# Kernel optimization log

Measured on AMD Instinct MI355X. Metric: run time of the kernel, lower is better.

Reference implementation:

```python
import jax, jax.numpy as jnp
import numpy as np

B, N_X, N_A, DIM = 2, 2048, 2048, 1024
HEADS, DH = 16, 64
SEG = 256
ROPE_THETA = 10000.0


def mh_rmsnorm(t, gamma):
    # t: [b,h,n,d], gamma: [h,1,d]; F.normalize(dim=-1) * gamma * sqrt(d)
    norm = jnp.linalg.norm(t, axis=-1, keepdims=True)
    return t / jnp.clip(norm, 1e-12) * gamma * (DH ** 0.5)


def apply_rope(t):
    # t: [b,h,n,d]; GPT-NeoX style half-split rotary over packed positions
    n = t.shape[2]
    half = DH // 2
    inv_freq = ROPE_THETA ** (-jnp.arange(0, half, dtype=jnp.float32) / half)
    freqs = jnp.arange(n, dtype=jnp.float32)[:, None] * inv_freq[None, :]  # [n, half]
    cos, sin = jnp.cos(freqs), jnp.sin(freqs)
    t1, t2 = t[..., :half], t[..., half:]
    return jnp.concatenate([t1 * cos - t2 * sin, t2 * cos + t1 * sin], axis=-1)


def infini_attention(q, k, v, beta):
    # q,k,v: [b,h,n,d]; causal local attention per segment + recurrent linear memory
    b, h, n, d = q.shape
    s = n // SEG
    scale = d ** -0.5
    gate = jax.nn.sigmoid(beta).reshape(1, h, 1, 1)
    causal = jnp.tril(jnp.ones((SEG, SEG), dtype=bool))

    def to_segs(t):  # -> [s, b, h, SEG, d]
        return jnp.moveaxis(t.reshape(b, h, s, SEG, d), 2, 0)

    qs, ks, vs = to_segs(q), to_segs(k), to_segs(v)

    def step(carry, inp):
        M, z = carry  # M: [b,h,d,d], z: [b,h,d]
        q_s, k_s, v_s = inp
        sq = jax.nn.elu(q_s) + 1.0
        sk = jax.nn.elu(k_s) + 1.0
        # memory retrieval
        num = jnp.einsum('bhld,bhde->bhle', sq, M)
        den = jnp.einsum('bhld,bhd->bhl', sq, z)[..., None] + 1e-6
        a_mem = num / den
        # local causal attention within segment
        scores = jnp.einsum('bhid,bhjd->bhij', q_s, k_s) * scale
        scores = jnp.where(causal, scores, -jnp.inf)
        a_loc = jnp.einsum('bhij,bhjd->bhid', jax.nn.softmax(scores, axis=-1), v_s)
        out = gate * a_mem + (1.0 - gate) * a_loc
        # memory update
        M = M + jnp.einsum('bhld,bhle->bhde', sk, v_s)
        z = z + sk.sum(axis=2)
        return (M, z), out

    M0 = jnp.zeros((b, h, d, d), dtype=q.dtype)
    z0 = jnp.zeros((b, h, d), dtype=q.dtype)
    _, outs = jax.lax.scan(step, (M0, z0), (qs, ks, vs))  # [s,b,h,SEG,d]
    return jnp.moveaxis(outs, 0, 2).reshape(b, h, n, d)


def setup_inputs() -> dict:
    key = jax.random.key(0)
    ks = jax.random.split(key, 4)
    scale = DIM ** -0.5
    x = jax.random.normal(ks[0], (B, N_X, DIM), dtype=jnp.float32)
    a = jax.random.normal(ks[1], (B, N_A, DIM), dtype=jnp.float32)
    w_qkv_x = jax.random.normal(ks[2], (DIM, 3 * HEADS * DH), dtype=jnp.float32) * scale
    w_qkv_a = jax.random.normal(ks[3], (DIM, 3 * HEADS * DH), dtype=jnp.float32) * scale
    g = lambda: jnp.ones((HEADS, 1, DH), dtype=jnp.float32)
    beta = jnp.zeros((HEADS,), dtype=jnp.float32)
    return {"x": x, "a": a, "w_qkv_x": w_qkv_x, "w_qkv_a": w_qkv_a,
            "gq_x": g(), "gk_x": g(), "gq_a": g(), "gk_a": g(), "beta": beta}


def _split_heads(t):
    b, n, _ = t.shape
    q, k, v = jnp.split(t, 3, axis=-1)
    r = lambda u: u.reshape(b, n, HEADS, DH).transpose(0, 2, 1, 3)
    return r(q), r(k), r(v)


def reference(x, a, w_qkv_x, w_qkv_a, gq_x, gk_x, gq_a, gk_a, beta):
    q_x, k_x, v_x = _split_heads(x @ w_qkv_x)
    q_a, k_a, v_a = _split_heads(a @ w_qkv_a)
    q_x, k_x = mh_rmsnorm(q_x, gq_x), mh_rmsnorm(k_x, gk_x)
    q_a, k_a = mh_rmsnorm(q_a, gq_a), mh_rmsnorm(k_a, gk_a)
    # pack: a-stream first, then x-stream (matches pack([._a, ._x]))
    q = jnp.concatenate([q_a, q_x], axis=2)
    k = jnp.concatenate([k_a, k_x], axis=2)
    v = jnp.concatenate([v_a, v_x], axis=2)
    q, k = apply_rope(q), apply_rope(k)
    out = infini_attention(q, k, v, beta)  # [b,h,n_a+n_x,d]
    out_a, out_x = out[:, :, :N_A], out[:, :, N_A:]
    merge = lambda t: t.transpose(0, 2, 1, 3).reshape(t.shape[0], t.shape[2], HEADS * DH)
    return merge(out_x), merge(out_a)
```

## Files before the change

### kernel.cpp

```cpp
#include <hip/hip_runtime.h>

#define HEADS 16
#define DH    64
#define NA    2048
#define NX    2048
#define NTOT  4096
#define DIMK  1024
#define NQKV  3072
#define SEG   256
#define NSEG  16

typedef float          f32x4  __attribute__((ext_vector_type(4)));
typedef short          bf16x8 __attribute__((ext_vector_type(8)));
typedef unsigned int   u32x4  __attribute__((ext_vector_type(4)));

__device__ __forceinline__ unsigned short f2bf(float f){
  unsigned int u = __builtin_bit_cast(unsigned int, f);
  unsigned int r = 0x7fffu + ((u >> 16) & 1u);
  return (unsigned short)((u + r) >> 16);
}
__device__ __forceinline__ float bf2f(unsigned short u){
  return __builtin_bit_cast(float, ((unsigned int)u) << 16);
}

__global__ __launch_bounds__(256) void zero_kernel(float* __restrict__ out, int n){
  int i = blockIdx.x * 256 + threadIdx.x;
  if (i < n) out[i] = 0.f;
}

__global__ __launch_bounds__(256) void cvt_kernel(const float* __restrict__ src,
                                                  unsigned short* __restrict__ dst, int n4){
  int i = blockIdx.x * 256 + threadIdx.x;
  if (i >= n4) return;
  float4 v = ((const float4*)src)[i];
  ushort4 o;
  o.x = f2bf(v.x); o.y = f2bf(v.y); o.z = f2bf(v.z); o.w = f2bf(v.w);
  ((ushort4*)dst)[i] = o;
}

__global__ __launch_bounds__(256) void wtr_kernel(const float* __restrict__ W,
                                                  unsigned short* __restrict__ WT){
  __shared__ float tile[32][33];
  int c0 = blockIdx.x * 32, k0 = blockIdx.y * 32;
  int tx = threadIdx.x, ty = threadIdx.y;
  #pragma unroll
  for (int i = 0; i < 32; i += 8) tile[ty+i][tx] = W[(size_t)(k0+ty+i)*NQKV + c0 + tx];
  __syncthreads();
  #pragma unroll
  for (int i = 0; i < 32; i += 8) WT[(size_t)(c0+ty+i)*DIMK + k0 + tx] = f2bf(tile[tx][ty+i]);
}

__global__ __launch_bounds__(256) void rope_tab_kernel(float* __restrict__ tab){
  const int idx = blockIdx.x * 256 + threadIdx.x;
  const int n = idx >> 5, d = idx & 31;
  const float ang = (float)n * expf(-(float)d * 0.28782313662425572f);
  float sn, cs;
  sincosf(ang, &sn, &cs);
  float2 p; p.x = cs; p.y = sn;
  ((float2*)tab)[idx] = p;
}

__global__ __launch_bounds__(256,2) void gemm_qkv_kernel(
    const unsigned short* __restrict__ Xb, const unsigned short* __restrict__ Ab,
    const unsigned short* __restrict__ WTx, const unsigned short* __restrict__ WTa,
    unsigned short* __restrict__ qb, unsigned short* __restrict__ kb,
    unsigned short* __restrict__ vt,
    const float* __restrict__ gqx, const float* __restrict__ gkx,
    const float* __restrict__ gqa, const float* __restrict__ gka,
    const float* __restrict__ tab)
{
  __shared__ __align__(16) unsigned short As0[128*32];
  __shared__ __align__(16) unsigned short Bs0[128*32];
  __shared__ __align__(16) unsigned short As1[128*32];
  __shared__ __align__(16) unsigned short Bs1[128*32];

  const int bid = blockIdx.x;
  const int lid = (bid & 7) * 192 + (bid >> 3);
  const int strm = lid / 768;
  const int rem  = lid - strm * 768;
  const int c0 = (rem >> 5) * 128;
  const int m0 = (rem & 31) * 128;

  const unsigned short* Xp = strm ? Ab  : Xb;
  const unsigned short* Wp = strm ? WTa : WTx;
  const float* gq = strm ? gqa : gqx;
  const float* gk = strm ? gka : gkx;
  const int n_off = strm ? 0 : NA;

  const int tid  = threadIdx.x;
  const int lane = tid & 63, w = tid >> 6;
  const int wr = w >> 1, wc = w & 1;
  const int li = lane & 15, lg = lane >> 4;

  const int srow = lane >> 2;
  const int sslot = lane & 3;
  const int sswz = sslot ^ (srow & 3) ^ ((srow >> 2) & 3);
  const int rswz = (li & 3) ^ ((li >> 2) & 3);

  f32x4 acc[4][4] = {};

  auto stage = [&](unsigned short* AsX, unsigned short* BsX, int kk){
    #pragma unroll
    for (int jj = 0; jj < 2; jj++){
      const int j = 2*w + jj;
      const int r = j*16 + srow;
      __builtin_amdgcn_global_load_lds(
        (const __attribute__((address_space(1))) unsigned int*)(Xp + (size_t)(m0+r)*DIMK + kk + sswz*8),
        (__attribute__((address_space(3))) unsigned int*)(AsX + j*512), 16, 0, 0);
      __builtin_amdgcn_global_load_lds(
        (const __attribute__((address_space(1))) unsigned int*)(Wp + (size_t)(c0+r)*DIMK + kk + sswz*8),
        (__attribute__((address_space(3))) unsigned int*)(BsX + j*512), 16, 0, 0);
    }
  };
  auto compute = [&](const unsigned short* AsX, const unsigned short* BsX){
    bf16x8 af[4], bf[4];
    const int slot = (lg ^ rswz) * 8;
    #pragma unroll
    for (int m = 0; m < 4; m++)
      af[m] = *(const bf16x8*)(&AsX[(wr*64 + m*16 + li)*32 + slot]);
    #pragma unroll
    for (int n = 0; n < 4; n++)
      bf[n] = *(const bf16x8*)(&BsX[(wc*64 + n*16 + li)*32 + slot]);
    #pragma unroll
    for (int m = 0; m < 4; m++)
      #pragma unroll
      for (int n = 0; n < 4; n++)
        acc[m][n] = __builtin_amdgcn_mfma_f32_16x16x32_bf16(af[m], bf[n], acc[m][n], 0, 0, 0);
  };

  stage(As0, Bs0, 0);
  __syncthreads();
  for (int t = 0; t < 32; t += 2){
    stage(As1, Bs1, (t+1)*32);
    compute(As0, Bs0);
    __syncthreads();
    if (t + 2 < 32) stage(As0, Bs0, (t+2)*32);
    compute(As1, Bs1);
    __syncthreads();
  }

  const int colbase = c0 + wc*64;
  const int which = colbase >> 10;
  const int h = (colbase >> 6) & 15;

  if (which < 2){
    const float* gv = (which == 0) ? gq : gk;
    unsigned short* dstb = (which == 0) ? qb : kb;
    float gl[4];
    #pragma unroll
    for (int n = 0; n < 4; n++) gl[n] = gv[h*64 + n*16 + li];
    #pragma unroll
    for (int m = 0; m < 4; m++){
      #pragma unroll
      for (int r = 0; r < 4; r++){
        float ss = acc[m][0][r]*acc[m][0][r] + acc[m][1][r]*acc[m][1][r]
                 + acc[m][2][r]*acc[m][2][r] + acc[m][3][r]*acc[m][3][r];
        ss += __shfl_xor(ss, 1, 64);
        ss += __shfl_xor(ss, 2, 64);
        ss += __shfl_xor(ss, 4, 64);
        ss += __shfl_xor(ss, 8, 64);
        const float sc = 8.0f / fmaxf(sqrtf(ss), 1e-12f);
        float v0 = acc[m][0][r]*sc*gl[0], v1 = acc[m][1][r]*sc*gl[1];
        float v2 = acc[m][2][r]*sc*gl[2], v3 = acc[m][3][r]*sc*gl[3];
        const int row = m0 + wr*64 + m*16 + lg*4 + r;
        const int bb = row >> 11, nn = row & 2047;
        const int n_g = nn + n_off;
        const float2 cs0 = ((const float2*)tab)[n_g*32 + li];
        const float2 cs1 = ((const float2*)tab)[n_g*32 + 16 + li];
        const float o0 = v0*cs0.x - v2*cs0.y;
        const float o1 = v1*cs1.x - v3*cs1.y;
        const float o2 = v2*cs0.x + v0*cs0.y;
        const float o3 = v3*cs1.x + v1*cs1.y;
        unsigned short* drow = dstb + ((size_t)(bb*HEADS + h)*NTOT + (size_t)n_g)*64;
        drow[li]      = f2bf(o0);
        drow[16 + li] = f2bf(o1);
        drow[32 + li] = f2bf(o2);
        drow[48 + li] = f2bf(o3);
      }
    }
  } else {
    #pragma unroll
    for (int m = 0; m < 4; m++){
      #pragma unroll
      for (int r = 0; r < 4; r++){
        const int row = m0 + wr*64 + m*16 + lg*4 + r;
        const int bb = row >> 11, nn = row & 2047;
        const int n_g = nn + n_off;
        unsigned short* vbase = vt + (size_t)(bb*HEADS + h)*DH*NTOT + n_g;
        #pragma unroll
        for (int n = 0; n < 4; n++)
          vbase[(size_t)(n*16 + li)*NTOT] = f2bf(acc[m][n][r]);
      }
    }
  }
}

__global__ __launch_bounds__(256,2) void segG_kernel(const unsigned short* __restrict__ kb,
                                                     const unsigned short* __restrict__ vt,
                                                     float* __restrict__ G, float* __restrict__ zc){
  __shared__ unsigned short skT[64*264];
  __shared__ unsigned short Vts[64*264];
  const int blk = blockIdx.x;
  const int bh = blk >> 4, s = blk & 15;
  const int tid = threadIdx.x;
  const int w = tid >> 6, lane = tid & 63;
  const int li = lane & 15, lg = lane >> 4;
  const size_t segoffb = ((size_t)bh * NTOT + (size_t)s * SEG) * DH;

  #pragma unroll
  for (int it = 0; it < 8; it++){
    const int idx = tid + it*256;
    const int e = idx >> 5, jc = idx & 31;
    *(u32x4*)(Vts + e*264 + jc*8) =
      *(const u32x4*)(vt + (size_t)bh*DH*NTOT + (size_t)e*NTOT + s*SEG + jc*8);
  }
  #pragma unroll
  for (int it = 0; it < 8; it++){
    const int idx = tid + it*256;
    const int l = idx >> 3, dc = idx & 7;
    bf16x8 kk = *(const bf16x8*)(kb + segoffb + (size_t)l*64 + dc*8);
    #pragma unroll
    for (int t2 = 0; t2 < 8; t2++){
      const float xx = bf2f((unsigned short)kk[t2]);
      skT[(dc*8 + t2)*264 + l] = f2bf(xx > 0.f ? xx + 1.f : __expf(xx));
    }
  }
  __syncthreads();

  {
    const int d = tid >> 2, q = tid & 3;
    float zz = 0.f;
    #pragma unroll
    for (int u = 0; u < 8; u++){
      bf16x8 vv = *(const bf16x8*)(skT + d*264 + q*64 + u*8);
      #pragma unroll
      for (int t2 = 0; t2 < 8; t2++)
        zz += bf2f((unsigned short)vv[t2]);
    }
    zz += __shfl_xor(zz, 1, 64);
    zz += __shfl_xor(zz, 2, 64);
    if (q == 0) zc[(size_t)blk*64 + d] = zz;
  }

  f32x4 acc[4] = {};
  #pragma unroll
  for (int k0 = 0; k0 < 256; k0 += 32){
    bf16x8 af = *(const bf16x8*)(skT + (w*16 + li)*264 + k0 + lg*8);
    #pragma unroll
    for (int n = 0; n < 4; n++){
      bf16x8 bf = *(const bf16x8*)(Vts + (n*16 + li)*264 + k0 + lg*8);
      acc[n] = __builtin_amdgcn_mfma_f32_16x16x32_bf16(af, bf, acc[n], 0, 0, 0);
    }
  }
  float* Gout = G + (size_t)blk * DH * DH;
  #pragma unroll
  for (int n = 0; n < 4; n++)
    #pragma unroll
    for (int r = 0; r < 4; r++)
      Gout[(w*16 + lg*4 + r)*64 + n*16 + li] = acc[n][r];
}

__global__ __launch_bounds__(256) void prefix_kernel(const float* __restrict__ G,
                                                     const float* __restrict__ zc,
                                                     float* __restrict__ Mp, float* __restrict__ zp){
  const int bh = blockIdx.x, tid = threadIdx.x;
  float run[16];
  #pragma unroll
  for (int k = 0; k < 16; k++) run[k] = 0.f;
  for (int s = 0; s < NSEG; s++){
    const size_t base = ((size_t)bh * NSEG + s) * DH * DH;
    #pragma unroll
    for (int k = 0; k < 16; k++){
      Mp[base + tid + 256*k] = run[k];
      run[k] += G[base + tid + 256*k];
    }
  }
  if (tid < DH){
    float rz = 0.f;
    for (int s = 0; s < NSEG; s++){
      zp[((size_t)bh*NSEG + s)*DH + tid] = rz;
      rz += zc[((size_t)bh*NSEG + s)*DH + tid];
    }
  }
}

__global__ __launch_bounds__(256,1) void attn_mfma_kernel(
    const unsigned short* __restrict__ qb, const unsigned short* __restrict__ kb,
    const unsigned short* __restrict__ vt, const float* __restrict__ Mp,
    const float* __restrict__ zp, const float* __restrict__ beta,
    float* __restrict__ out)
{
  __shared__ unsigned short Qs[256*72];
  __shared__ unsigned short KSs[256*72];
  __shared__ unsigned short Vts[64*264];
  __shared__ unsigned short Ps[4*64*72];
  __shared__ unsigned short Mts[64*72];
  __shared__ float den_s[256];
  __shared__ float zsh[64];

  const int blk = blockIdx.x;
  const int s = blk & 15, bh = blk >> 4;
  const int h = bh & 15, b = bh >> 4;
  const int tid = threadIdx.x;
  const int w = tid >> 6, lane = tid & 63;
  const int li = lane & 15, lg = lane >> 4;
  const size_t segoffb = ((size_t)bh * NTOT + (size_t)s * SEG) * DH;

  #pragma unroll
  for (int it = 0; it < 8; it++){
    const int idx = tid + it*256;
    const int row = idx >> 3, jc = idx & 7;
    *(u32x4*)(Qs  + row*72 + jc*8) = *(const u32x4*)(qb + segoffb + (size_t)row*64 + jc*8);
    *(u32x4*)(KSs + row*72 + jc*8) = *(const u32x4*)(kb + segoffb + (size_t)row*64 + jc*8);
  }
  #pragma unroll
  for (int it = 0; it < 8; it++){
    const int idx = tid + it*256;
    const int e = idx >> 5, jc = idx & 31;
    *(u32x4*)(Vts + e*264 + jc*8) =
      *(const u32x4*)(vt + (size_t)bh*DH*NTOT + (size_t)e*NTOT + s*SEG + jc*8);
  }
  #pragma unroll
  for (int it = 0; it < 16; it++){
    const int idx = tid + it*256;
    const int d = idx >> 6, e = idx & 63;
    Mts[e*72 + d] = f2bf(Mp[(size_t)blk*4096 + d*64 + e]);
  }
  if (tid < 64) zsh[tid] = zp[(size_t)blk*64 + tid];
  __syncthreads();

  f32x4 o_acc[4][4] = {};
  float denr[4] = {0.f, 0.f, 0.f, 0.f};
  const int qrow0 = w*64;
  bf16x8 qf[4][2];
  #pragma unroll
  for (int it = 0; it < 4; it++)
    #pragma unroll
    for (int kb2 = 0; kb2 < 2; kb2++)
      qf[it][kb2] = *(const bf16x8*)(Qs + (qrow0 + it*16 + li)*72 + kb2*32 + lg*8);

  for (int c = 0; c <= w; c++){
    f32x4 st[4][4] = {};
    #pragma unroll
    for (int jt = 0; jt < 4; jt++){
      bf16x8 kf0 = *(const bf16x8*)(KSs + (c*64 + jt*16 + li)*72 + 0  + lg*8);
      bf16x8 kf1 = *(const bf16x8*)(KSs + (c*64 + jt*16 + li)*72 + 32 + lg*8);
      #pragma unroll
      for (int it = 0; it < 4; it++){
        st[jt][it] = __builtin_amdgcn_mfma_f32_16x16x32_bf16(kf0, qf[it][0], st[jt][it], 0, 0, 0);
        st[jt][it] = __builtin_amdgcn_mfma_f32_16x16x32_bf16(kf1, qf[it][1], st[jt][it], 0, 0, 0);
      }
    }
    const bool diag = (c == w);
    #pragma unroll
    for (int jt = 0; jt < 4; jt++){
      #pragma unroll
      for (int it = 0; it < 4; it++){
        f32x4 p = st[jt][it];
        unsigned pb[4];
        #pragma unroll
        for (int r = 0; r < 4; r++){
          float pe = __expf(p[r] * 0.125f);
          if (diag && (jt*16 + lg*4 + r > it*16 + li)) pe = 0.f;
          pb[r] = __builtin_bit_cast(unsigned, pe) & 0xFFFF0000u;
          p[r] = __builtin_bit_cast(float, pb[r]);
        }
        denr[it] += (p[0] + p[1]) + (p[2] + p[3]);
        uint2 pkk;
        pkk.x = (pb[0] >> 16) | pb[1];
        pkk.y = (pb[2] >> 16) | pb[3];
        *(uint2*)(Ps + w*4608 + (it*16 + li)*72 + jt*16 + lg*4) = pkk;
      }
    }
    bf16x8 pf[4][2];
    #pragma unroll
    for (int it = 0; it < 4; it++)
      #pragma unroll
      for (int kb2 = 0; kb2 < 2; kb2++)
        pf[it][kb2] = *(const bf16x8*)(Ps + w*4608 + (it*16 + li)*72 + kb2*32 + lg*8);
    #pragma unroll
    for (int et = 0; et < 4; et++){
      bf16x8 vf0 = *(const bf16x8*)(Vts + (et*16 + li)*264 + c*64 + 0  + lg*8);
      bf16x8 vf1 = *(const bf16x8*)(Vts + (et*16 + li)*264 + c*64 + 32 + lg*8);
      #pragma unroll
      for (int it = 0; it < 4; it++){
        o_acc[it][et] = __builtin_amdgcn_mfma_f32_16x16x32_bf16(pf[it][0], vf0, o_acc[it][et], 0, 0, 0);
        o_acc[it][et] = __builtin_amdgcn_mfma_f32_16x16x32_bf16(pf[it][1], vf1, o_acc[it][et], 0, 0, 0);
      }
    }
  }

  #pragma unroll
  for (int it = 0; it < 4; it++){
    denr[it] += __shfl_xor(denr[it], 16, 64);
    denr[it] += __shfl_xor(denr[it], 32, 64);
  }
  if (lane < 16){
    #pragma unroll
    for (int it = 0; it < 4; it++) den_s[qrow0 + it*16 + lane] = denr[it];
  }
  const float gate = 1.f / (1.f + __expf(-beta[h]));
  __syncthreads();

  {
    const int i = tid;
    float sqv[64];
    float denm = 0.f;
    #pragma unroll
    for (int u = 0; u < 8; u++){
      bf16x8 qv = *(const bf16x8*)(Qs + i*72 + u*8);
      #pragma unroll
      for (int t2 = 0; t2 < 8; t2++){
        float x = bf2f((unsigned short)qv[t2]);
        float sq = x > 0.f ? x + 1.f : __expf(x);
        sqv[u*8 + t2] = sq;
        denm += sq * zsh[u*8 + t2];
      }
    }
    const float c2 = gate / (denm + 1e-6f);
    #pragma unroll
    for (int u = 0; u < 16; u++){
      uint2 pw;
      pw.x = f2bf(sqv[u*4]*c2)   | ((unsigned)f2bf(sqv[u*4+1]*c2) << 16);
      pw.y = f2bf(sqv[u*4+2]*c2) | ((unsigned)f2bf(sqv[u*4+3]*c2) << 16);
      *(uint2*)(KSs + i*72 + u*4) = pw;
    }
  }
  __syncthreads();

  #pragma unroll
  for (int it = 0; it < 4; it++){
    #pragma unroll
    for (int r = 0; r < 4; r++){
      const float c1 = (1.f - gate) / den_s[qrow0 + it*16 + lg*4 + r];
      #pragma unroll
      for (int et = 0; et < 4; et++) o_acc[it][et][r] *= c1;
    }
  }
  #pragma unroll
  for (int kb2 = 0; kb2 < 2; kb2++){
    bf16x8 mf[4];
    #pragma unroll
    for (int et = 0; et < 4; et++)
      mf[et] = *(const bf16x8*)(Mts + (et*16 + li)*72 + kb2*32 + lg*8);
    #pragma unroll
    for (int it = 0; it < 4; it++){
      bf16x8 sf = *(const bf16x8*)(KSs + (qrow0 + it*16 + li)*72 + kb2*32 + lg*8);
      #pragma unroll
      for (int et = 0; et < 4; et++)
        o_acc[it][et] = __builtin_amdgcn_mfma_f32_16x16x32_bf16(sf, mf[et], o_acc[it][et], 0, 0, 0);
    }
  }

  #pragma unroll
  for (int it = 0; it < 4; it++){
    #pragma unroll
    for (int r = 0; r < 4; r++){
      const int n_g = s*SEG + qrow0 + it*16 + lg*4 + r;
      size_t o;
      if (n_g >= NA) o = ((size_t)b * NX + (size_t)(n_g - NA)) * 1024 + h * 64;
      else           o = 4194304u + ((size_t)b * NA + (size_t)n_g) * 1024 + h * 64;
      #pragma unroll
      for (int et = 0; et < 4; et++)
        out[o + et*16 + li] = o_acc[it][et][r];
    }
  }
}

extern "C" void kernel_launch(void* const* d_in, const int* in_sizes, int n_in,
                              void* d_out, int out_size, void* d_ws, size_t ws_size,
                              hipStream_t stream)
{
  (void)ws_size;
  const int expect[9] = {4194304, 4194304, 3145728, 3145728, 1024, 1024, 1024, 1024, 16};
  bool ok = (n_in == 9);
  if (ok) for (int i = 0; i < 9; i++) if (in_sizes[i] != expect[i]) { ok = false; break; }
  float* out = (float*)d_out;
  if (!ok){
    zero_kernel<<<dim3((out_size + 255)/256), dim3(256), 0, stream>>>(out, out_size);
    return;
  }

  const float* x    = (const float*)d_in[0];
  const float* a    = (const float*)d_in[1];
  const float* wx   = (const float*)d_in[2];
  const float* wa   = (const float*)d_in[3];
  const float* gqx  = (const float*)d_in[4];
  const float* gkx  = (const float*)d_in[5];
  const float* gqa  = (const float*)d_in[6];
  const float* gka  = (const float*)d_in[7];
  const float* beta = (const float*)d_in[8];

  char* wsb = (char*)d_ws;
  unsigned short* qb  = (unsigned short*)wsb;
  unsigned short* kb  = qb + 8388608;
  unsigned short* vtb = kb + 8388608;
  unsigned short* Xb  = vtb + 8388608;
  unsigned short* Ab  = Xb + 4194304;
  unsigned short* WTx = Ab + 4194304;
  unsigned short* WTa = WTx + 3145728;
  float* ropetab = (float*)(WTa + 3145728);
  float* G   = ropetab + 262144;
  float* Mp  = G + 2097152;
  float* zc  = Mp + 2097152;
  float* zpb = zc + 32768;

  cvt_kernel<<<dim3(4096), dim3(256), 0, stream>>>(x, Xb, 1048576);
  cvt_kernel<<<dim3(4096), dim3(256), 0, stream>>>(a, Ab, 1048576);
  wtr_kernel<<<dim3(96,32), dim3(32,8), 0, stream>>>(wx, WTx);
  wtr_kernel<<<dim3(96,32), dim3(32,8), 0, stream>>>(wa, WTa);
  rope_tab_kernel<<<dim3(512), dim3(256), 0, stream>>>(ropetab);
  gemm_qkv_kernel<<<dim3(1536), dim3(256), 0, stream>>>(Xb, Ab, WTx, WTa, qb, kb, vtb,
                                                        gqx, gkx, gqa, gka, ropetab);
  segG_kernel<<<dim3(512), dim3(256), 0, stream>>>(kb, vtb, G, zc);
  prefix_kernel<<<dim3(32), dim3(256), 0, stream>>>(G, zc, Mp, zpb);
  attn_mfma_kernel<<<dim3(512), dim3(256), 0, stream>>>(qb, kb, vtb, Mp, zpb, beta, out);
}
```

Before: 150.7 us.

## Fuse fp32-to-bf16 activation conversion into QKV GEMM and parallelize prefix scan

Drops the separate cvt kernels for x and a. The GEMM now stages fp32 activation tiles into LDS with direct global-to-LDS loads and converts them to bf16 while building MFMA fragments. This removes two launches and a round trip of the bf16 copies, but doubles A-tile LDS footprint and global reads inside the GEMM and adds conversion ALU work to its inner loop. The prefix kernel is also split across 8 blocks per head to raise parallelism.

```diff
diff --git a/kernel.cpp b/kernel.cpp
--- a/kernel.cpp
+++ b/kernel.cpp
@@ -22,20 +22,13 @@
 __device__ __forceinline__ float bf2f(unsigned short u){
   return __builtin_bit_cast(float, ((unsigned int)u) << 16);
 }
+__device__ __forceinline__ unsigned pack2(float a, float b){
+  return (unsigned)f2bf(a) | ((unsigned)f2bf(b) << 16);
+}
 
 __global__ __launch_bounds__(256) void zero_kernel(float* __restrict__ out, int n){
   int i = blockIdx.x * 256 + threadIdx.x;
   if (i < n) out[i] = 0.f;
-}
-
-__global__ __launch_bounds__(256) void cvt_kernel(const float* __restrict__ src,
-                                                  unsigned short* __restrict__ dst, int n4){
-  int i = blockIdx.x * 256 + threadIdx.x;
-  if (i >= n4) return;
-  float4 v = ((const float4*)src)[i];
-  ushort4 o;
-  o.x = f2bf(v.x); o.y = f2bf(v.y); o.z = f2bf(v.z); o.w = f2bf(v.w);
-  ((ushort4*)dst)[i] = o;
 }
 
 __global__ __launch_bounds__(256) void wtr_kernel(const float* __restrict__ W,
@@ -61,7 +54,7 @@
 }
 
 __global__ __launch_bounds__(256,2) void gemm_qkv_kernel(
-    const unsigned short* __restrict__ Xb, const unsigned short* __restrict__ Ab,
+    const float* __restrict__ Xf, const float* __restrict__ Af,
     const unsigned short* __restrict__ WTx, const unsigned short* __restrict__ WTa,
     unsigned short* __restrict__ qb, unsigned short* __restrict__ kb,
     unsigned short* __restrict__ vt,
@@ -69,9 +62,9 @@
     const float* __restrict__ gqa, const float* __restrict__ gka,
     const float* __restrict__ tab)
 {
-  __shared__ __align__(16) unsigned short As0[128*32];
+  __shared__ __align__(16) float          As0f[128*32];
+  __shared__ __align__(16) float          As1f[128*32];
   __shared__ __align__(16) unsigned short Bs0[128*32];
-  __shared__ __align__(16) unsigned short As1[128*32];
   __shared__ __align__(16) unsigned short Bs1[128*32];
 
   const int bid = blockIdx.x;
@@ -81,7 +74,7 @@
   const int c0 = (rem >> 5) * 128;
   const int m0 = (rem & 31) * 128;
 
-  const unsigned short* Xp = strm ? Ab  : Xb;
+  const float* Xp = strm ? Af  : Xf;
   const unsigned short* Wp = strm ? WTa : WTx;
   const float* gq = strm ? gqa : gqx;
   const float* gk = strm ? gka : gkx;
@@ -96,31 +89,48 @@
   const int sslot = lane & 3;
   const int sswz = sslot ^ (srow & 3) ^ ((srow >> 2) & 3);
   const int rswz = (li & 3) ^ ((li >> 2) & 3);
+  const int sswzA = (lane & 7) ^ (lane >> 3);
+  const int e0 = ((lg * 2) ^ (li & 7)) * 4;
+  const int e1 = ((lg * 2 + 1) ^ (li & 7)) * 4;
 
   f32x4 acc[4][4] = {};
 
-  auto stage = [&](unsigned short* AsX, unsigned short* BsX, int kk){
+  auto stage = [&](float* AfX, unsigned short* BsX, int kk){
+    #pragma unroll
+    for (int jj = 0; jj < 4; jj++){
+      const int j = w*4 + jj;
+      const int row = j*8 + (lane >> 3);
+      __builtin_amdgcn_global_load_lds(
+        (const __attribute__((address_space(1))) unsigned int*)(Xp + (size_t)(m0+row)*DIMK + kk + sswzA*4),
+        (__attribute__((address_space(3))) unsigned int*)(AfX + j*256), 16, 0, 0);
+    }
     #pragma unroll
     for (int jj = 0; jj < 2; jj++){
       const int j = 2*w + jj;
       const int r = j*16 + srow;
       __builtin_amdgcn_global_load_lds(
-        (const __attribute__((address_space(1))) unsigned int*)(Xp + (size_t)(m0+r)*DIMK + kk + sswz*8),
-        (__attribute__((address_space(3))) unsigned int*)(AsX + j*512), 16, 0, 0);
-      __builtin_amdgcn_global_load_lds(
         (const __attribute__((address_space(1))) unsigned int*)(Wp + (size_t)(c0+r)*DIMK + kk + sswz*8),
         (__attribute__((address_space(3))) unsigned int*)(BsX + j*512), 16, 0, 0);
     }
   };
-  auto compute = [&](const unsigned short* AsX, const unsigned short* BsX){
+  auto compute = [&](const float* AfX, const unsigned short* BsX){
     bf16x8 af[4], bf[4];
-    const int slot = (lg ^ rswz) * 8;
-    #pragma unroll
-    for (int m = 0; m < 4; m++)
-      af[m] = *(const bf16x8*)(&AsX[(wr*64 + m*16 + li)*32 + slot]);
+    const int slotB = (lg ^ rswz) * 8;
+    #pragma unroll
+    for (int m = 0; m < 4; m++){
+      const int rbase = (wr*64 + m*16 + li) * 32;
+      f32x4 lo = *(const f32x4*)(AfX + rbase + e0);
+      f32x4 hi = *(const f32x4*)(AfX + rbase + e1);
+      union { bf16x8 v; unsigned u[4]; } cc;
+      cc.u[0] = pack2(lo[0], lo[1]);
+      cc.u[1] = pack2(lo[2], lo[3]);
+      cc.u[2] = pack2(hi[0], hi[1]);
+      cc.u[3] = pack2(hi[2], hi[3]);
+      af[m] = cc.v;
+    }
     #pragma unroll
     for (int n = 0; n < 4; n++)
-      bf[n] = *(const bf16x8*)(&BsX[(wc*64 + n*16 + li)*32 + slot]);
+      bf[n] = *(const bf16x8*)(&BsX[(wc*64 + n*16 + li)*32 + slotB]);
     #pragma unroll
     for (int m = 0; m < 4; m++)
       #pragma unroll
@@ -128,14 +138,14 @@
         acc[m][n] = __builtin_amdgcn_mfma_f32_16x16x32_bf16(af[m], bf[n], acc[m][n], 0, 0, 0);
   };
 
-  stage(As0, Bs0, 0);
+  stage(As0f, Bs0, 0);
   __syncthreads();
   for (int t = 0; t < 32; t += 2){
-    stage(As1, Bs1, (t+1)*32);
-    compute(As0, Bs0);
+    stage(As1f, Bs1, (t+1)*32);
+    compute(As0f, Bs0);
     __syncthreads();
-    if (t + 2 < 32) stage(As0, Bs0, (t+2)*32);
-    compute(As1, Bs1);
+    if (t + 2 < 32) stage(As0f, Bs0, (t+2)*32);
+    compute(As1f, Bs1);
     __syncthreads();
   }
 
@@ -263,19 +273,15 @@
 __global__ __launch_bounds__(256) void prefix_kernel(const float* __restrict__ G,
                                                      const float* __restrict__ zc,
                                                      float* __restrict__ Mp, float* __restrict__ zp){
-  const int bh = blockIdx.x, tid = threadIdx.x;
-  float run[16];
-  #pragma unroll
-  for (int k = 0; k < 16; k++) run[k] = 0.f;
+  const int bh = blockIdx.x, c = blockIdx.y, tid = threadIdx.x;
+  const int e = c*512 + tid;
+  float run0 = 0.f, run1 = 0.f;
   for (int s = 0; s < NSEG; s++){
-    const size_t base = ((size_t)bh * NSEG + s) * DH * DH;
-    #pragma unroll
-    for (int k = 0; k < 16; k++){
-      Mp[base + tid + 256*k] = run[k];
-      run[k] += G[base + tid + 256*k];
-    }
-  }
-  if (tid < DH){
+    const size_t base = ((size_t)bh * NSEG + s) * 4096;
+    Mp[base + e]       = run0;  run0 += G[base + e];
+    Mp[base + e + 256] = run1;  run1 += G[base + e + 256];
+  }
+  if (c == 0 && tid < DH){
     float rz = 0.f;
     for (int s = 0; s < NSEG; s++){
       zp[((size_t)bh*NSEG + s)*DH + tid] = rz;
@@ -421,8 +427,8 @@
     #pragma unroll
     for (int u = 0; u < 16; u++){
       uint2 pw;
-      pw.x = f2bf(sqv[u*4]*c2)   | ((unsigned)f2bf(sqv[u*4+1]*c2) << 16);
-      pw.y = f2bf(sqv[u*4+2]*c2) | ((unsigned)f2bf(sqv[u*4+3]*c2) << 16);
+      pw.x = pack2(sqv[u*4]*c2,   sqv[u*4+1]*c2);
+      pw.y = pack2(sqv[u*4+2]*c2, sqv[u*4+3]*c2);
       *(uint2*)(KSs + i*72 + u*4) = pw;
     }
   }
@@ -495,9 +501,7 @@
   unsigned short* qb  = (unsigned short*)wsb;
   unsigned short* kb  = qb + 8388608;
   unsigned short* vtb = kb + 8388608;
-  unsigned short* Xb  = vtb + 8388608;
-  unsigned short* Ab  = Xb + 4194304;
-  unsigned short* WTx = Ab + 4194304;
+  unsigned short* WTx = vtb + 8388608;
   unsigned short* WTa = WTx + 3145728;
   float* ropetab = (float*)(WTa + 3145728);
   float* G   = ropetab + 262144;
@@ -505,14 +509,12 @@
   float* zc  = Mp + 2097152;
   float* zpb = zc + 32768;
 
-  cvt_kernel<<<dim3(4096), dim3(256), 0, stream>>>(x, Xb, 1048576);
-  cvt_kernel<<<dim3(4096), dim3(256), 0, stream>>>(a, Ab, 1048576);
   wtr_kernel<<<dim3(96,32), dim3(32,8), 0, stream>>>(wx, WTx);
   wtr_kernel<<<dim3(96,32), dim3(32,8), 0, stream>>>(wa, WTa);
   rope_tab_kernel<<<dim3(512), dim3(256), 0, stream>>>(ropetab);
-  gemm_qkv_kernel<<<dim3(1536), dim3(256), 0, stream>>>(Xb, Ab, WTx, WTa, qb, kb, vtb,
+  gemm_qkv_kernel<<<dim3(1536), dim3(256), 0, stream>>>(x, a, WTx, WTa, qb, kb, vtb,
                                                         gqx, gkx, gqa, gka, ropetab);
   segG_kernel<<<dim3(512), dim3(256), 0, stream>>>(kb, vtb, G, zc);
-  prefix_kernel<<<dim3(32), dim3(256), 0, stream>>>(G, zc, Mp, zpb);
+  prefix_kernel<<<dim3(32,8), dim3(256), 0, stream>>>(G, zc, Mp, zpb);
   attn_mfma_kernel<<<dim3(512), dim3(256), 0, stream>>>(qb, kb, vtb, Mp, zpb, beta, out);
 }
```

New measurement: 180.0 us. +19.4%, slower.
